# Optimization experiments

Hardware: AMD Instinct MI355X
Metric: run time of the kernel (lower is better)

## Reference

```python
import jax, jax.numpy as jnp
import numpy as np

N, IN_F, OUT_F, H = 4096, 256, 64, 8


def setup_inputs() -> dict:
    key = jax.random.key(0)
    k1, k2, k3, k4 = jax.random.split(key, 4)
    features = jax.random.normal(k1, (N, IN_F), dtype=jnp.float32)
    adj_matrix = jax.random.randint(k2, (N, N), 0, 2, dtype=jnp.int32)
    # xavier_uniform bounds
    bw = float(np.sqrt(6.0 / (IN_F + OUT_F)))
    W = jax.random.uniform(k3, (IN_F, OUT_F), dtype=jnp.float32, minval=-bw, maxval=bw)
    ba = float(np.sqrt(6.0 / (2 * OUT_F + 1)))
    attention = jax.random.uniform(k4, (H, 2 * OUT_F, 1), dtype=jnp.float32, minval=-ba, maxval=ba)
    return {"features": features, "adj_matrix": adj_matrix, "W": W, "attention": attention}


def reference(features, adj_matrix, W, attention):
    h = features @ W                      # [N, F]
    F = h.shape[1]
    a_src = attention[:, :F, 0]           # [H, F] (dotted with row node h_i)
    a_dst = attention[:, F:, 0]           # [H, F] (dotted with col node h_j)
    # score[h,i,j] = <concat(h_i, h_j), a_h> = src[h,i] + dst[h,j]
    src = jnp.einsum('nf,hf->hn', h, a_src)   # [H, N]
    dst = jnp.einsum('nf,hf->hn', h, a_dst)   # [H, N]
    scores = src[:, :, None] + dst[:, None, :]           # [H, N, N]
    NEG = jnp.float32(-9e15)
    scores = jnp.where(adj_matrix[None, :, :] > 0, scores, NEG)
    alpha = jax.nn.softmax(scores, axis=-1)               # [H, N, N]
    alpha = jnp.mean(alpha, axis=0)                       # [N, N] (mean over heads)
    return alpha @ h                                      # [N, F]
```

## Files before the change

kernel.cpp:

```cpp
#include <hip/hip_runtime.h>
#include <hip/hip_bf16.h>

#define NN   4096
#define INF_ 256
#define OUTF 64
#define NH   8
#define HSTR 72
#define NPAD 576

using bf16x8 = __attribute__((ext_vector_type(8))) short;
using f32x4  = __attribute__((ext_vector_type(4))) float;

__device__ __forceinline__ void gload_lds16(const void* g, void* l) {
  __builtin_amdgcn_global_load_lds((__attribute__((address_space(1))) void*)(g),
                                   (__attribute__((address_space(3))) void*)(l),
                                   16, 0, 0);
}

__device__ __forceinline__ unsigned short f2bf(float x) {
  unsigned u = __float_as_uint(x);
  unsigned r = (u + 0x7FFFu + ((u >> 16) & 1u)) >> 16;
  return (unsigned short)r;
}

__global__ __launch_bounds__(256) void k_prep(const float* __restrict__ feat,
                                              const float* __restrict__ W,
                                              const float* __restrict__ att,
                                              unsigned short* __restrict__ Gt) {
  __shared__ float fl[16][INF_];
  __shared__ float hl[16][65];
  __shared__ float el[NH][16];
  int j0 = blockIdx.x * 16;
  int tid = threadIdx.x;
  const float4* src = (const float4*)(feat + (size_t)j0 * INF_);
  for (int i = tid; i < 16 * 64; i += 256) {
    int r = i >> 6, c4 = i & 63;
    *(float4*)&fl[r][c4 * 4] = src[i];
  }
  __syncthreads();
  int c  = tid & 63;
  int rg = tid >> 6;
  float acc[4] = {0.f, 0.f, 0.f, 0.f};
#pragma unroll 8
  for (int k = 0; k < INF_; ++k) {
    float w = W[k * OUTF + c];
#pragma unroll
    for (int m = 0; m < 4; ++m) acc[m] = fmaf(fl[rg * 4 + m][k], w, acc[m]);
  }
#pragma unroll
  for (int m = 0; m < 4; ++m) hl[rg * 4 + m][c] = acc[m];
  __syncthreads();
  if (tid < NH * 16) {
    int hh = tid >> 4, row = tid & 15;
    float d = 0.f;
#pragma unroll 8
    for (int f = 0; f < 64; ++f) d = fmaf(hl[row][f], att[hh * 128 + 64 + f], d);
    el[hh][row] = expf(d);
  }
  __syncthreads();
  for (int i = tid; i < NPAD * 8; i += 256) {
    int u = i & 7, cc = i >> 3;
    int j2 = u * 2;
    int hh2 = cc / HSTR, c2 = cc - hh2 * HSTR;
    float e0 = el[hh2][j2], e1 = el[hh2][j2 + 1];
    float v0, v1;
    if (c2 < 64)      { v0 = e0 * hl[j2][c2]; v1 = e1 * hl[j2 + 1][c2]; }
    else if (c2 == 64){ v0 = e0;              v1 = e1; }
    else              { v0 = 0.f;             v1 = 0.f; }
    ushort2 o; o.x = f2bf(v0); o.y = f2bf(v1);
    *(ushort2*)&Gt[(size_t)cc * NN + j0 + j2] = o;
  }
}

#define BM 128
#define BN 64
#define BK 64
#define KS 4
#define NT (NN / (KS * BK))
#define NTILE (NPAD / BN)
#define MTILE (NN / BM)

#define WAITVM2()  asm volatile("s_waitcnt vmcnt(2)" ::: "memory")
#define WAITVM10() asm volatile("s_waitcnt vmcnt(10)" ::: "memory")
#define WAITVM0()  asm volatile("s_waitcnt vmcnt(0)" ::: "memory")
#define WAITLGKM() asm volatile("s_waitcnt lgkmcnt(0)" ::: "memory")
#define BAR()      asm volatile("s_barrier" ::: "memory")

__global__ __launch_bounds__(256, 4) void k_gemm(const int* __restrict__ adj,
                                                 const unsigned short* __restrict__ B,
                                                 float* __restrict__ Cp) {
  __shared__ alignas(16) unsigned short As[BM * BK];
  __shared__ alignas(16) unsigned short Bs[2][BN * BK];

  const int nwg = NTILE * MTILE * KS;
  const int cpx = nwg >> 3;
  int id  = blockIdx.x;
  int wg  = (id & 7) * cpx + (id >> 3);
  int nt  = wg % NTILE;
  int mt  = (wg / NTILE) % MTILE;
  int ks  = wg / (NTILE * MTILE);

  int m0 = mt * BM, n0 = nt * BN, k0 = ks * (NT * BK);
  int tid = threadIdx.x;
  int lane = tid & 63, wid = tid >> 6;
  int wm = wid >> 1, wn = wid & 1;
  f32x4 acc[4][2] = {};

  int arow = tid >> 3;
  int agrp = tid & 7;
  int aswz = agrp ^ (arow & 7);
  const int* Ag = adj + (size_t)(m0 + arow) * NN + k0 + agrp * 8;
  unsigned adst = (unsigned)arow * BK + (unsigned)aswz * 8;

  const unsigned short* Bg = B + (size_t)(n0 + arow) * NN + k0 + aswz * 8;
  unsigned ldsB = (unsigned)(wid * 8) * BK;

  int4 ra[4][2];

#define ALOAD(kt_)                                                            \
  do {                                                                        \
    _Pragma("unroll") for (int q = 0; q < 4; ++q) {                           \
      const int4* p = (const int4*)(Ag + (size_t)(q * 32) * NN + (kt_) * BK); \
      ra[q][0] = p[0]; ra[q][1] = p[1];                                       \
    }                                                                         \
  } while (0)

#define AWRITE()                                                              \
  do {                                                                        \
    _Pragma("unroll") for (int q = 0; q < 4; ++q) {                           \
      unsigned w0 = (unsigned)(ra[q][0].x | (ra[q][0].y << 16)) * 0x3F80u;    \
      unsigned w1 = (unsigned)(ra[q][0].z | (ra[q][0].w << 16)) * 0x3F80u;    \
      unsigned w2 = (unsigned)(ra[q][1].x | (ra[q][1].y << 16)) * 0x3F80u;    \
      unsigned w3 = (unsigned)(ra[q][1].z | (ra[q][1].w << 16)) * 0x3F80u;    \
      uint4 wv = make_uint4(w0, w1, w2, w3);                                  \
      *(uint4*)&As[adst + (unsigned)(q * 32 * BK)] = wv;                      \
    }                                                                         \
  } while (0)

#define BSTAGE(b, kt_)                                                        \
  do {                                                                        \
    _Pragma("unroll") for (int i = 0; i < 2; ++i)                             \
      gload_lds16(Bg + (size_t)(i * 32) * NN + (kt_) * BK,                    \
                  &Bs[b][ldsB + i * 32 * BK]);                                \
  } while (0)

  ALOAD(0);
  BSTAGE(0, 0);

  int hi = lane >> 4, r15 = lane & 15, x7 = lane & 7;

  for (int kt = 0; kt < NT; ++kt) {
    int cur = kt & 1;
    WAITVM2();
    BAR();
    AWRITE();
    if (kt + 1 < NT) {
      ALOAD(kt + 1);
      BSTAGE(cur ^ 1, kt + 1);
      WAITVM10();
    } else {
      WAITVM0();
    }
    WAITLGKM();
    BAR();
#pragma unroll
    for (int kk = 0; kk < 2; ++kk) {
      bf16x8 af[4], bfr[2];
#pragma unroll
      for (int m = 0; m < 4; ++m) {
        int row = wm * 64 + m * 16 + r15;
        af[m] = *(const bf16x8*)&As[row * BK + (((kk * 4 + hi) ^ x7) * 8)];
      }
#pragma unroll
      for (int n = 0; n < 2; ++n) {
        int row = wn * 32 + n * 16 + r15;
        bfr[n] = *(const bf16x8*)&Bs[cur][row * BK + (((kk * 4 + hi) ^ x7) * 8)];
      }
#pragma unroll
      for (int m = 0; m < 4; ++m)
#pragma unroll
        for (int n = 0; n < 2; ++n)
          acc[m][n] = __builtin_amdgcn_mfma_f32_16x16x32_bf16(af[m], bfr[n], acc[m][n], 0, 0, 0);
    }
  }

  float* Cout = Cp + (size_t)ks * NN * NPAD;
#pragma unroll
  for (int m = 0; m < 4; ++m)
#pragma unroll
    for (int n = 0; n < 2; ++n)
#pragma unroll
      for (int j = 0; j < 4; ++j) {
        int row = m0 + wm * 64 + m * 16 + (lane >> 4) * 4 + j;
        int col = n0 + wn * 32 + n * 16 + (lane & 15);
        Cout[(size_t)row * NPAD + col] = acc[m][n][j];
      }
#undef ALOAD
#undef AWRITE
#undef BSTAGE
}

__global__ __launch_bounds__(256) void k_epi(const float* __restrict__ Cp,
                                             float* __restrict__ out) {
  int idx = blockIdx.x * 256 + threadIdx.x;
  int i = idx >> 6, f = idx & 63;
  const float* row = Cp + (size_t)i * NPAD;
  const size_t stride = (size_t)NN * NPAD;
  float s = 0.f;
#pragma unroll
  for (int hh = 0; hh < NH; ++hh) {
    float num = 0.f, den = 0.f;
#pragma unroll
    for (int ks = 0; ks < KS; ++ks) {
      num += row[ks * stride + hh * HSTR + f];
      den += row[ks * stride + hh * HSTR + 64];
    }
    float inv = (den > 0.f) ? (1.f / den) : 0.f;
    s = fmaf(num, inv, s);
  }
  out[idx] = 0.125f * s;
}

extern "C" void kernel_launch(void* const* d_in, const int* in_sizes, int n_in,
                              void* d_out, int out_size, void* d_ws, size_t ws_size,
                              hipStream_t stream) {
  const float* feat = (const float*)d_in[0];
  const int*   adj  = (const int*)d_in[1];
  const float* W    = (const float*)d_in[2];
  const float* att  = (const float*)d_in[3];
  float* out = (float*)d_out;

  const size_t GT_B = (size_t)NPAD * NN * 2;
  char* ws = (char*)d_ws;
  unsigned short* Gt = (unsigned short*)(ws);
  float*          Cp = (float*)(ws + GT_B);

  k_prep<<<NN / 16, 256, 0, stream>>>(feat, W, att, Gt);
  k_gemm<<<NTILE * MTILE * KS, 256, 0, stream>>>(adj, Gt, Cp);
  k_epi <<<NN * OUTF / 256, 256, 0, stream>>>(Cp, out);
}
```

Before: 69.22 us.

## Widen GEMM N-tile to 96 and deepen A/B prefetch to two stages

Raises the B tile width from 64 to 96 columns, so there are 6 N-tiles instead of 9 and each adjacency A tile is re-read fewer times. It also moves from double to triple-buffered B staging in LDS, with two A register sets, so loads run two k-steps ahead. The loop is hand-unrolled with fixed vmcnt waits. In exchange it uses more registers and LDS, drops the occupancy hint from 4 to 3 workgroups, and the hardcoded wait counts are fragile.

```diff
diff --git a/kernel.cpp b/kernel.cpp
--- a/kernel.cpp
+++ b/kernel.cpp
@@ -73,29 +73,27 @@
 }
 
 #define BM 128
-#define BN 64
+#define BN 96
 #define BK 64
 #define KS 4
-#define NT (NN / (KS * BK))
-#define NTILE (NPAD / BN)
-#define MTILE (NN / BM)
-
-#define WAITVM2()  asm volatile("s_waitcnt vmcnt(2)" ::: "memory")
-#define WAITVM10() asm volatile("s_waitcnt vmcnt(10)" ::: "memory")
-#define WAITVM0()  asm volatile("s_waitcnt vmcnt(0)" ::: "memory")
+#define NT 16
+#define NTILE 6
+#define MTILE 32
+#define BSZ (BN * BK)
+
+#define SEP()      asm volatile("" ::: "memory")
+#define WAITVM(N)  asm volatile("s_waitcnt vmcnt(" #N ")" ::: "memory")
 #define WAITLGKM() asm volatile("s_waitcnt lgkmcnt(0)" ::: "memory")
 #define BAR()      asm volatile("s_barrier" ::: "memory")
 
-__global__ __launch_bounds__(256, 4) void k_gemm(const int* __restrict__ adj,
-                                                 const unsigned short* __restrict__ B,
+__global__ __launch_bounds__(256, 3) void k_gemm(const int* __restrict__ adj,
+                                                 const unsigned short* __restrict__ Bsrc,
                                                  float* __restrict__ Cp) {
   __shared__ alignas(16) unsigned short As[BM * BK];
-  __shared__ alignas(16) unsigned short Bs[2][BN * BK];
-
-  const int nwg = NTILE * MTILE * KS;
-  const int cpx = nwg >> 3;
+  __shared__ alignas(16) unsigned short BsF[3 * BSZ];
+
   int id  = blockIdx.x;
-  int wg  = (id & 7) * cpx + (id >> 3);
+  int wg  = (id & 7) * (768 >> 3) + (id >> 3);
   int nt  = wg % NTILE;
   int mt  = (wg / NTILE) % MTILE;
   int ks  = wg / (NTILE * MTILE);
@@ -104,7 +102,7 @@
   int tid = threadIdx.x;
   int lane = tid & 63, wid = tid >> 6;
   int wm = wid >> 1, wn = wid & 1;
-  f32x4 acc[4][2] = {};
+  f32x4 acc[4][3] = {};
 
   int arow = tid >> 3;
   int agrp = tid & 7;
@@ -112,92 +110,90 @@
   const int* Ag = adj + (size_t)(m0 + arow) * NN + k0 + agrp * 8;
   unsigned adst = (unsigned)arow * BK + (unsigned)aswz * 8;
 
-  const unsigned short* Bg = B + (size_t)(n0 + arow) * NN + k0 + aswz * 8;
-  unsigned ldsB = (unsigned)(wid * 8) * BK;
-
-  int4 ra[4][2];
-
-#define ALOAD(kt_)                                                            \
-  do {                                                                        \
-    _Pragma("unroll") for (int q = 0; q < 4; ++q) {                           \
-      const int4* p = (const int4*)(Ag + (size_t)(q * 32) * NN + (kt_) * BK); \
-      ra[q][0] = p[0]; ra[q][1] = p[1];                                       \
-    }                                                                         \
+  const unsigned short* Bg = Bsrc + (size_t)(n0 + arow) * NN + k0 + aswz * 8;
+
+  int4 ra0[4][2], ra1[4][2];
+
+#define ALOAD(RA, KOFF)                                                       \
+  do { _Pragma("unroll") for (int q = 0; q < 4; ++q) {                        \
+    const int4* p = (const int4*)(Ag + (size_t)(q * 32) * NN + (KOFF));       \
+    RA[q][0] = p[0]; RA[q][1] = p[1]; } } while (0)
+
+#define AWRITE(RA)                                                            \
+  do { _Pragma("unroll") for (int q = 0; q < 4; ++q) {                        \
+    unsigned w0 = (unsigned)(RA[q][0].x | (RA[q][0].y << 16)) * 0x3F80u;      \
+    unsigned w1 = (unsigned)(RA[q][0].z | (RA[q][0].w << 16)) * 0x3F80u;      \
+    unsigned w2 = (unsigned)(RA[q][1].x | (RA[q][1].y << 16)) * 0x3F80u;      \
+    unsigned w3 = (unsigned)(RA[q][1].z | (RA[q][1].w << 16)) * 0x3F80u;      \
+    *(uint4*)&As[adst + (unsigned)(q * 32 * BK)] = make_uint4(w0, w1, w2, w3);\
+  } } while (0)
+
+#define BSTAGE(BIO, KOFF)                                                     \
+  do { _Pragma("unroll") for (int r = 0; r < 3; ++r)                          \
+    gload_lds16(Bg + (size_t)(r * 32) * NN + (KOFF),                          \
+                &BsF[(unsigned)(BIO) + (unsigned)((r * 32 + wid * 8) * BK)]); \
   } while (0)
 
-#define AWRITE()                                                              \
-  do {                                                                        \
-    _Pragma("unroll") for (int q = 0; q < 4; ++q) {                           \
-      unsigned w0 = (unsigned)(ra[q][0].x | (ra[q][0].y << 16)) * 0x3F80u;    \
-      unsigned w1 = (unsigned)(ra[q][0].z | (ra[q][0].w << 16)) * 0x3F80u;    \
-      unsigned w2 = (unsigned)(ra[q][1].x | (ra[q][1].y << 16)) * 0x3F80u;    \
-      unsigned w3 = (unsigned)(ra[q][1].z | (ra[q][1].w << 16)) * 0x3F80u;    \
-      uint4 wv = make_uint4(w0, w1, w2, w3);                                  \
-      *(uint4*)&As[adst + (unsigned)(q * 32 * BK)] = wv;                      \
-    }                                                                         \
-  } while (0)
-
-#define BSTAGE(b, kt_)                                                        \
-  do {                                                                        \
-    _Pragma("unroll") for (int i = 0; i < 2; ++i)                             \
-      gload_lds16(Bg + (size_t)(i * 32) * NN + (kt_) * BK,                    \
-                  &Bs[b][ldsB + i * 32 * BK]);                                \
-  } while (0)
-
-  ALOAD(0);
-  BSTAGE(0, 0);
-
   int hi = lane >> 4, r15 = lane & 15, x7 = lane & 7;
 
-  for (int kt = 0; kt < NT; ++kt) {
-    int cur = kt & 1;
-    WAITVM2();
-    BAR();
-    AWRITE();
-    if (kt + 1 < NT) {
-      ALOAD(kt + 1);
-      BSTAGE(cur ^ 1, kt + 1);
-      WAITVM10();
-    } else {
-      WAITVM0();
-    }
-    WAITLGKM();
-    BAR();
-#pragma unroll
-    for (int kk = 0; kk < 2; ++kk) {
-      bf16x8 af[4], bfr[2];
-#pragma unroll
-      for (int m = 0; m < 4; ++m) {
-        int row = wm * 64 + m * 16 + r15;
-        af[m] = *(const bf16x8*)&As[row * BK + (((kk * 4 + hi) ^ x7) * 8)];
-      }
-#pragma unroll
-      for (int n = 0; n < 2; ++n) {
-        int row = wn * 32 + n * 16 + r15;
-        bfr[n] = *(const bf16x8*)&Bs[cur][row * BK + (((kk * 4 + hi) ^ x7) * 8)];
-      }
-#pragma unroll
-      for (int m = 0; m < 4; ++m)
-#pragma unroll
-        for (int n = 0; n < 2; ++n)
-          acc[m][n] = __builtin_amdgcn_mfma_f32_16x16x32_bf16(af[m], bfr[n], acc[m][n], 0, 0, 0);
-    }
-  }
+#define COMPUTE(BCO)                                                          \
+  do { _Pragma("unroll") for (int kk = 0; kk < 2; ++kk) {                     \
+    bf16x8 af[4], bfr[3];                                                     \
+    _Pragma("unroll") for (int m = 0; m < 4; ++m)                             \
+      af[m] = *(const bf16x8*)&As[(wm * 64 + m * 16 + r15) * BK +             \
+                                  (((kk * 4 + hi) ^ x7) * 8)];                \
+    _Pragma("unroll") for (int n = 0; n < 3; ++n)                             \
+      bfr[n] = *(const bf16x8*)&BsF[(unsigned)(BCO) +                         \
+                                    (unsigned)((wn * 48 + n * 16 + r15) * BK) \
+                                    + (unsigned)(((kk * 4 + hi) ^ x7) * 8)];  \
+    _Pragma("unroll") for (int m = 0; m < 4; ++m)                             \
+      _Pragma("unroll") for (int n = 0; n < 3; ++n)                           \
+        acc[m][n] = __builtin_amdgcn_mfma_f32_16x16x32_bf16(af[m], bfr[n],    \
+                                                            acc[m][n], 0,0,0);\
+  } } while (0)
+
+#define GITER(RA, WA, DOI, WB)                                                \
+  WA;                                                                         \
+  WAITLGKM();                                                                 \
+  BAR();                                                                      \
+  AWRITE(RA);                                                                 \
+  if (DOI) { ALOAD(RA, koff); SEP(); BSTAGE(bio, koff); }                     \
+  WB;                                                                         \
+  WAITLGKM();                                                                 \
+  BAR();                                                                      \
+  COMPUTE(bco);                                                               \
+  bco += BSZ; if (bco == 3 * BSZ) bco = 0;                                    \
+  bio += BSZ; if (bio == 3 * BSZ) bio = 0;
+
+  ALOAD(ra0, 0);  SEP();  BSTAGE(0, 0);    SEP();
+  ALOAD(ra1, BK); SEP();  BSTAGE(BSZ, BK); SEP();
+
+  int bco = 0, bio = 2 * BSZ;
+  int koff = 2 * BK;
+
+  for (int kt2 = 0; kt2 < 7; ++kt2) {
+    GITER(ra0, WAITVM(14), 1, WAITVM(22)); koff += BK;
+    GITER(ra1, WAITVM(14), 1, WAITVM(22)); koff += BK;
+  }
+  GITER(ra0, WAITVM(14), 0, WAITVM(11));
+  GITER(ra1, WAITVM(3), 0, WAITVM(0));
 
   float* Cout = Cp + (size_t)ks * NN * NPAD;
 #pragma unroll
   for (int m = 0; m < 4; ++m)
 #pragma unroll
-    for (int n = 0; n < 2; ++n)
+    for (int n = 0; n < 3; ++n)
 #pragma unroll
       for (int j = 0; j < 4; ++j) {
-        int row = m0 + wm * 64 + m * 16 + (lane >> 4) * 4 + j;
-        int col = n0 + wn * 32 + n * 16 + (lane & 15);
+        int row = m0 + wm * 64 + m * 16 + hi * 4 + j;
+        int col = n0 + wn * 48 + n * 16 + r15;
         Cout[(size_t)row * NPAD + col] = acc[m][n][j];
       }
 #undef ALOAD
 #undef AWRITE
 #undef BSTAGE
+#undef COMPUTE
+#undef GITER
 }
 
 __global__ __launch_bounds__(256) void k_epi(const float* __restrict__ Cp,
```

New measurement: 80.00 us. 1.16x slower.
